# Optimization experiments

Hardware: AMD Instinct MI355X
Metric: run time of the kernel (lower is better)

Reference implementation:

```python
import jax, jax.numpy as jnp
import numpy as np
from jax import lax

B = 1024
D_VQ = 64
KS = 1024
KX = 1024
BETA = 0.25


def _conv1d(x, w, b):
    # x: [N, Cin, L], w: [Cout, Cin, 3], 'same' padding
    y = lax.conv_general_dilated(x, w, (1,), [(1, 1)], dimension_numbers=('NCH', 'OIH', 'NCH'))
    return y + b[None, :, None]


def _conv2d(x, w, b):
    # x: [N, Cin, H, W], w: [Cout, Cin, 3, 3], 'same' padding
    y = lax.conv_general_dilated(x, w, (1, 1), [(1, 1), (1, 1)], dimension_numbers=('NCHW', 'OIHW', 'NCHW'))
    return y + b[None, :, None, None]


def _gelu(x):
    return jax.nn.gelu(x, approximate=False)


def _vq_ema(z_e, codebook, beta):
    # z_e: [N, D], codebook: [K, D]
    d = (jnp.sum(z_e * z_e, axis=1, keepdims=True)
         - 2.0 * (z_e @ codebook.T)
         + jnp.sum(codebook * codebook, axis=1)[None, :])  # [N, K]
    idx = jnp.argmin(d, axis=1)                              # [N]
    z_q = codebook[idx]                                      # gather [N, D]
    vq_loss = beta * jnp.mean((z_e - lax.stop_gradient(z_q)) ** 2)
    z_q_st = z_e + lax.stop_gradient(z_q - z_e)              # straight-through
    n = z_e.shape[0]
    probs = jnp.zeros((codebook.shape[0],), z_e.dtype).at[idx].add(1.0) / n
    perplexity = jnp.exp(-jnp.sum(probs * jnp.log(probs + 1e-10)))
    return z_q_st, idx, vq_loss, perplexity


def setup_inputs() -> dict:
    key = jax.random.key(0)
    ks = iter(jax.random.split(key, 40))

    def p(shape, s=0.05):
        return jax.random.normal(next(ks), shape, jnp.float32) * s

    inp = {
        'cubes': jax.random.normal(next(ks), (B, 9, 8, 72), jnp.float32),
        # spectral encoder
        's_w1': p((16, 1, 3)), 's_b1': jnp.zeros((16,), jnp.float32),
        's_w2': p((16, 16, 3)), 's_b2': jnp.zeros((16,), jnp.float32),
        's_fc_w': p((D_VQ, 16 * 8)), 's_fc_b': jnp.zeros((D_VQ,), jnp.float32),
        'cb_s': p((KS, D_VQ), 1.0),
        # spectral decoder
        's_dec_fc_w': p((16 * 8, D_VQ)), 's_dec_fc_b': jnp.zeros((16 * 8,), jnp.float32),
        's_dec_w1': p((16, 16, 3)), 's_dec_b1': jnp.zeros((16,), jnp.float32),
        's_dec_w2': p((1, 16, 3)), 's_dec_b2': jnp.zeros((1,), jnp.float32),
        # spatial encoder
        'x_w1': p((16, 8, 3, 3)), 'x_b1': jnp.zeros((16,), jnp.float32),
        'x_w2': p((16, 16, 3, 3)), 'x_b2': jnp.zeros((16,), jnp.float32),
        'x_fc_w': p((D_VQ, 16 * 3 * 3)), 'x_fc_b': jnp.zeros((D_VQ,), jnp.float32),
        'cb_x': p((KX, D_VQ), 1.0),
        # spatial decoder
        'x_dec_fc_w': p((16 * 3 * 3, D_VQ)), 'x_dec_fc_b': jnp.zeros((16 * 3 * 3,), jnp.float32),
        'x_dec_w1': p((16, 16, 3, 3)), 'x_dec_b1': jnp.zeros((16,), jnp.float32),
        'x_dec_w2': p((8, 16, 3, 3)), 'x_dec_b2': jnp.zeros((8,), jnp.float32),
        'return_recon': 1,
    }
    return inp


def reference(cubes, s_w1, s_b1, s_w2, s_b2, s_fc_w, s_fc_b, cb_s,
              s_dec_fc_w, s_dec_fc_b, s_dec_w1, s_dec_b1, s_dec_w2, s_dec_b2,
              x_w1, x_b1, x_w2, x_b2, x_fc_w, x_fc_b, cb_x,
              x_dec_fc_w, x_dec_fc_b, x_dec_w1, x_dec_b1, x_dec_w2, x_dec_b2,
              return_recon):
    b, p, t, f = cubes.shape
    n = b * p * t
    c6 = cubes.reshape(b, p, t, 8, 3, 3)                   # [B,P,T,8,3,3]
    cperm = jnp.transpose(c6, (0, 1, 2, 4, 5, 3))          # [B,P,T,3,3,8]

    # --- spectral path ---
    spec = jnp.mean(cperm, axis=(3, 4))                    # [B,P,T,8]
    spec_seq = spec.reshape(n, 1, 8)
    s = _gelu(_conv1d(spec_seq, s_w1, s_b1))
    s = _gelu(_conv1d(s, s_w2, s_b2))
    z_e_s = s.reshape(n, 16 * 8) @ s_fc_w.T + s_fc_b       # [N,D]
    z_q_s, k_idx, vq_loss_s, perplex_s = _vq_ema(z_e_s, cb_s, BETA)
    emb_s = z_q_s.reshape(b, p, t, D_VQ)
    k_idx = k_idx.reshape(b, p, t)

    # --- spatial path ---
    spatial = c6.reshape(n, 8, 3, 3)
    x = _gelu(_conv2d(spatial, x_w1, x_b1))
    x = _gelu(_conv2d(x, x_w2, x_b2))
    z_e_x = x.reshape(n, 16 * 9) @ x_fc_w.T + x_fc_b
    z_q_x, m_idx, vq_loss_x, perplex_x = _vq_ema(z_e_x, cb_x, BETA)
    emb_x = z_q_x.reshape(b, p, t, D_VQ)
    m_idx = m_idx.reshape(b, p, t)

    total = vq_loss_s + vq_loss_x

    if return_recon:
        s_dec = (z_q_s @ s_dec_fc_w.T + s_dec_fc_b).reshape(n, 16, 8)
        s_dec = _gelu(_conv1d(s_dec, s_dec_w1, s_dec_b1))
        recon_s = _conv1d(s_dec, s_dec_w2, s_dec_b2)[:, 0, :].reshape(b, p, t, 8)
        recon_loss_s = jnp.mean((recon_s - spec) ** 2)

        x_dec = (z_q_x @ x_dec_fc_w.T + x_dec_fc_b).reshape(n, 16, 3, 3)
        x_dec = _gelu(_conv2d(x_dec, x_dec_w1, x_dec_b1))
        recon_x = _conv2d(x_dec, x_dec_w2, x_dec_b2)        # [N,8,3,3]
        recon_loss_x = jnp.mean((recon_x - spatial) ** 2)
        recon_loss_total = recon_loss_s + recon_loss_x
    else:
        recon_loss_total = jnp.float32(0.0)

    return (emb_s, emb_x, k_idx, m_idx, total, perplex_s, perplex_x, recon_loss_total)
```

## Files before the change

### kernel.cpp

```cpp
#include <hip/hip_runtime.h>
#include <math.h>

#define NTOK 73728

__device__ __forceinline__ float gelu_f(float x) {
    return 0.5f * x * (1.0f + erff(x * 0.70710678118654752440f));
}

__global__ void __launch_bounds__(256) k_prep(
    const float* __restrict__ cb_s, const float* __restrict__ cb_x,
    double* __restrict__ cn_s, double* __restrict__ cn_x,
    const float* __restrict__ s_dw1, const float* __restrict__ s_db1,
    const float* __restrict__ s_dfcw, const float* __restrict__ s_dfcb,
    float* __restrict__ weffT_s, float* __restrict__ beff_s,
    const float* __restrict__ x_dw1, const float* __restrict__ x_db1,
    const float* __restrict__ x_dfcw, const float* __restrict__ x_dfcb,
    float* __restrict__ weffT_x, float* __restrict__ beff_x,
    const float* __restrict__ s_fcw, float* __restrict__ fcwT_s,
    const float* __restrict__ x_fcw, float* __restrict__ fcwT_x,
    const float* __restrict__ s_w2, float* __restrict__ sw2T,
    const float* __restrict__ x_w1, float* __restrict__ xw1T,
    const float* __restrict__ x_w2, float* __restrict__ xw2T,
    const float* __restrict__ x_dw2, float* __restrict__ xdw2T)
{
// ... 60 lines not shown
            beff_x[o] = (float)bb;
        }
    } else if (bid < 108) {
        int i = (bid - 76) * 256 + tid;
        fcwT_s[i] = s_fcw[(i & 63) * 128 + (i >> 6)];
    } else if (bid < 144) {
        int i = (bid - 108) * 256 + tid;
        fcwT_x[i] = x_fcw[(i & 63) * 144 + (i >> 6)];
    } else {
        int i = (bid - 144) * 256 + tid;
        if (i < 768) {
            int c = i & 15, r = i >> 4;
            int ci = r / 3, dd = r % 3;
            sw2T[i] = s_w2[(c * 16 + ci) * 3 + dd];
        } else if (i < 1920) {
            int j = i - 768;
            int c = j & 15, r = j >> 4;
            int ci = r / 9, tap = r % 9;
            xw1T[j] = x_w1[(c * 8 + ci) * 9 + tap];
        } else if (i < 4224) {
            int j = i - 1920;
            int c = j & 15, r = j >> 4;
            int ci = r / 9, tap = r % 9;
            xw2T[j] = x_w2[(c * 16 + ci) * 9 + tap];
        } else {
            int j = i - 4224;
            int co = j & 7, r = j >> 3;
            int ci = r / 9, tap = r % 9;
            xdw2T[j] = x_dw2[(co * 16 + ci) * 9 + tap];
        }
    }
}

__global__ void __launch_bounds__(256) k_enc(
    const float* __restrict__ cubes,
    const float* __restrict__ s_w1, const float* __restrict__ s_b1,
    const float* __restrict__ sw2T, const float* __restrict__ s_b2,
    const float* __restrict__ fcwT_s, const float* __restrict__ s_fcb,
    float* __restrict__ emb_s,
    const float* __restrict__ xw1T, const float* __restrict__ x_b1,
    const float* __restrict__ xw2T, const float* __restrict__ x_b2,
    const float* __restrict__ fcwT_x, const float* __restrict__ x_fcb,
    float* __restrict__ emb_x)
{
    __shared__ float U[6528];
    int tid = threadIdx.x;
    int t = tid >> 4, c = tid & 15;
    if (blockIdx.x < 4608) {
        int b = blockIdx.x;
        float* S = U;
        float* A = U + 128;
        float* Bb = U + 2304;
        if (tid < 128) {
            int tk = tid >> 3, f = tid & 7;
            const float* cu = cubes + ((size_t)b * 16 + tk) * 72 + f * 9;
            float s = 0.f;
            #pragma unroll
            for (int k = 0; k < 9; ++k) s += cu[k];
            S[tk * 8 + f] = s * (1.0f / 9.0f);
        }
        __syncthreads();
        {
            float s0[8];
            *(float4*)&s0[0] = *(const float4*)&S[t * 8];
            *(float4*)&s0[4] = *(const float4*)&S[t * 8 + 4];
            float wa = s_w1[c * 3 + 0], wb = s_w1[c * 3 + 1], wc = s_w1[c * 3 + 2], bb = s_b1[c];
            #pragma unroll
            for (int l = 0; l < 8; ++l) {
                float v = fmaf(wb, s0[l], bb);
                if (l > 0) v = fmaf(wa, s0[l - 1], v);
                if (l < 7) v = fmaf(wc, s0[l + 1], v);
                A[t * 136 + c * 8 + l] = gelu_f(v);
            }
        }
        __syncthreads();
        {
            float acc[8];
            #pragma unroll
            for (int l = 0; l < 8; ++l) acc[l] = s_b2[c];
            for (int ci = 0; ci < 16; ++ci) {
                float r[8];
                *(float4*)&r[0] = *(const float4*)&A[t * 136 + ci * 8];
                *(float4*)&r[4] = *(const float4*)&A[t * 136 + ci * 8 + 4];
                float wa = sw2T[(ci * 3 + 0) * 16 + c];
                float wb = sw2T[(ci * 3 + 1) * 16 + c];
                float wc = sw2T[(ci * 3 + 2) * 16 + c];
                #pragma unroll
                for (int l = 0; l < 8; ++l) {
                    if (l > 0) acc[l] = fmaf(wa, r[l - 1], acc[l]);
                    acc[l] = fmaf(wb, r[l], acc[l]);
                    if (l < 7) acc[l] = fmaf(wc, r[l + 1], acc[l]);
                }
            }
            #pragma unroll
            for (int l = 0; l < 8; ++l) Bb[t * 136 + c * 8 + l] = gelu_f(acc[l]);
        }
        __syncthreads();
        {
            float4 zv = make_float4(s_fcb[c * 4 + 0], s_fcb[c * 4 + 1], s_fcb[c * 4 + 2], s_fcb[c * 4 + 3]);
            #pragma unroll 4
            for (int e = 0; e < 128; ++e) {
                float be = Bb[t * 136 + e];
                float4 wv = *(const float4*)(fcwT_s + (e << 6) + (c << 2));
                zv.x = fmaf(wv.x, be, zv.x);
                zv.y = fmaf(wv.y, be, zv.y);
                zv.z = fmaf(wv.z, be, zv.z);
                zv.w = fmaf(wv.w, be, zv.w);
            }
            *(float4*)(emb_s + ((size_t)b * 16 + t) * 64 + c * 4) = zv;
        }
    } else {
        int b = blockIdx.x - 4608;
        float* A = U;
        float* Bb = U + 3200;
        for (int u = tid; u < 1152; u += 256) {
            int tk = u / 72, e = u - tk * 72;
            int ci = e / 9, p = e - ci * 9;
            A[tk * 200 + ci * 12 + p] = cubes[(size_t)b * 1152 + u];
        }
        __syncthreads();
        {
            float acc[9];
            #pragma unroll
            for (int p = 0; p < 9; ++p) acc[p] = x_b1[c];
            for (int ci = 0; ci < 8; ++ci) {
                float r[12];
                *(float4*)&r[0] = *(const float4*)&A[t * 200 + ci * 12];
                *(float4*)&r[4] = *(const float4*)&A[t * 200 + ci * 12 + 4];
                *(float4*)&r[8] = *(const float4*)&A[t * 200 + ci * 12 + 8];
                float wv[9];
                #pragma unroll
                for (int q = 0; q < 9; ++q) wv[q] = xw1T[(ci * 9 + q) * 16 + c];
                #pragma unroll
                for (int p = 0; p < 9; ++p) {
                    int i = p / 3, j = p % 3;
                    #pragma unroll
                    for (int di = 0; di < 3; ++di) {
                        int ii = i + di - 1; if (ii < 0 || ii > 2) continue;
                        #pragma unroll
                        for (int dj = 0; dj < 3; ++dj) {
                            int jj = j + dj - 1; if (jj < 0 || jj > 2) continue;
                            acc[p] = fmaf(wv[di * 3 + dj], r[ii * 3 + jj], acc[p]);
                        }
                    }
                }
            }
            #pragma unroll
            for (int p = 0; p < 9; ++p) Bb[t * 200 + c * 12 + p] = gelu_f(acc[p]);
        }
        __syncthreads();
        {
            float acc[9];
            #pragma unroll
            for (int p = 0; p < 9; ++p) acc[p] = x_b2[c];
            for (int ci = 0; ci < 16; ++ci) {
                float r[12];
                *(float4*)&r[0] = *(const float4*)&Bb[t * 200 + ci * 12];
                *(float4*)&r[4] = *(const float4*)&Bb[t * 200 + ci * 12 + 4];
                *(float4*)&r[8] = *(const float4*)&Bb[t * 200 + ci * 12 + 8];
                float wv[9];
                #pragma unroll
                for (int q = 0; q < 9; ++q) wv[q] = xw2T[(ci * 9 + q) * 16 + c];
                #pragma unroll
                for (int p = 0; p < 9; ++p) {
                    int i = p / 3, j = p % 3;
                    #pragma unroll
                    for (int di = 0; di < 3; ++di) {
                        int ii = i + di - 1; if (ii < 0 || ii > 2) continue;
                        #pragma unroll
                        for (int dj = 0; dj < 3; ++dj) {
                            int jj = j + dj - 1; if (jj < 0 || jj > 2) continue;
                            acc[p] = fmaf(wv[di * 3 + dj], r[ii * 3 + jj], acc[p]);
                        }
                    }
                }
            }
            __syncthreads();
            #pragma unroll
            for (int p = 0; p < 9; ++p) A[t * 200 + c * 12 + p] = gelu_f(acc[p]);
        }
        __syncthreads();
        {
            float4 zv = make_float4(x_fcb[c * 4 + 0], x_fcb[c * 4 + 1], x_fcb[c * 4 + 2], x_fcb[c * 4 + 3]);
            #pragma unroll 4
            for (int e = 0; e < 144; ++e) {
                int ci = e / 9, p = e - ci * 9;
                float be = A[t * 200 + ci * 12 + p];
                float4 wv = *(const float4*)(fcwT_x + (e << 6) + (c << 2));
                zv.x = fmaf(wv.x, be, zv.x);
                zv.y = fmaf(wv.y, be, zv.y);
                zv.z = fmaf(wv.z, be, zv.z);
                zv.w = fmaf(wv.w, be, zv.w);
            }
            *(float4*)(emb_x + ((size_t)b * 16 + t) * 64 + c * 4) = zv;
        }
    }
}

__global__ void __launch_bounds__(256) k_vq(
    float* __restrict__ emb_s, float* __restrict__ emb_x,
    const float* __restrict__ cb_s, const float* __restrict__ cb_x,
    const double* __restrict__ cn_s, const double* __restrict__ cn_x,
    float* __restrict__ kidx, float* __restrict__ midx,
    int* __restrict__ hist_s, int* __restrict__ hist_x,
    double* __restrict__ p_vq_s, double* __restrict__ p_vq_x)
{
    __shared__ double pbest[4][64];
    __shared__ int pidx[4][64];
    __shared__ int lh[1024];
    int blk = blockIdx.x;
    int path = (blk >= 1152) ? 1 : 0;
    int b = blk - (path << 10) - (path << 7);
    float* emb = path ? emb_x : emb_s;
    const float* cb = path ? cb_x : cb_s;
    const double* cn = path ? cn_x : cn_s;
    float* idx_out = path ? midx : kidx;
    int* hist = path ? hist_x : hist_s;
    double* partial = path ? p_vq_x : p_vq_s;

    int tid = threadIdx.x;
    int w = tid >> 6, l = tid & 63;
    for (int u = tid; u < 1024; u += 256) lh[u] = 0;
    size_t n = (size_t)b * 64 + l;
    float z[64];
    {
        const float4* zp = (const float4*)(emb + n * 64);
        #pragma unroll
        for (int k = 0; k < 16; ++k) *(float4*)&z[k * 4] = zp[k];
    }
    int base = __builtin_amdgcn_readfirstlane(w << 8);
    const float* crb = cb + ((size_t)base << 6);
    const double* cnb = cn + base;
    double best = 1e300; int bi = base;
    for (int cc = 0; cc < 256; ++cc) {
        const float* cr = crb + (cc << 6);
        float d0 = 0.f, d1 = 0.f, d2 = 0.f, d3 = 0.f;
        #pragma unroll
        for (int k = 0; k < 64; k += 4) {
            d0 = fmaf(z[k + 0], cr[k + 0], d0);
            d1 = fmaf(z[k + 1], cr[k + 1], d1);
            d2 = fmaf(z[k + 2], cr[k + 2], d2);
            d3 = fmaf(z[k + 3], cr[k + 3], d3);
        }
        float dot = (d0 + d1) + (d2 + d3);
        double dd = cnb[cc] - 2.0 * (double)dot;
        if (dd < best) { best = dd; bi = base + cc; }
    }
    pbest[w][l] = best; pidx[w][l] = bi;
    __syncthreads();
    if (w == 0) {
        double bB = pbest[0][l]; int bj = pidx[0][l];
        #pragma unroll
        for (int q = 1; q < 4; ++q) {
            double d = pbest[q][l];
            if (d < bB) { bB = d; bj = pidx[q][l]; }
        }
        idx_out[n] = (float)bj;
        float qv[64];
        {
            const float4* cq = (const float4*)(cb + ((size_t)bj << 6));
            #pragma unroll
            for (int k = 0; k < 16; ++k) *(float4*)&qv[k * 4] = cq[k];
        }
        float vs = 0.f;
        #pragma unroll
        for (int k = 0; k < 64; ++k) { float df = z[k] - qv[k]; vs = fmaf(df, df, vs); }
        float4* zo = (float4*)(emb + n * 64);
        #pragma unroll
        for (int k = 0; k < 16; ++k) zo[k] = *(float4*)&qv[k * 4];
        atomicAdd(&lh[bj], 1);
        double s = (double)vs;
        #pragma unroll
        for (int o = 32; o > 0; o >>= 1) s += __shfl_down(s, o);
        if (l == 0) partial[b] = s;
    }
    __syncthreads();
    for (int u = tid; u < 1024; u += 256) if (lh[u] > 0) atomicAdd(&hist[u], lh[u]);
}

__global__ void __launch_bounds__(256) k_dec(
    const float* __restrict__ emb_s, const float* __restrict__ emb_x,
    const float* __restrict__ cubes,
    const float* __restrict__ weffT_s, const float* __restrict__ beff_s,
    const float* __restrict__ s_dw2, const float* __restrict__ s_db2,
    const float* __restrict__ weffT_x, const float* __restrict__ beff_x,
    const float* __restrict__ xdw2T, const float* __restrict__ x_db2,
    double* __restrict__ p_rec_s, double* __restrict__ p_rec_x)
{
    __shared__ float U[6016];
    __shared__ double wred[4];
    int tid = threadIdx.x;
    int t = tid >> 4, c = tid & 15;
    if (blockIdx.x < 4608) {
        int b = blockIdx.x;
        float* Z = U;
        float* Bb = U + 1152;
        float* S = U + 3328;
        {
            int tk = tid >> 4, dq = tid & 15;
            *(float4*)&Z[tk * 72 + dq * 4] =
                *(const float4*)(emb_s + (size_t)b * 1024 + (size_t)tid * 4);
        }
        if (tid < 128) {
            int tk = tid >> 3, f = tid & 7;
            const float* cu = cubes + ((size_t)b * 16 + tk) * 72 + f * 9;
            float s = 0.f;
            #pragma unroll
            for (int k = 0; k < 9; ++k) s += cu[k];
            S[tk * 8 + f] = s * (1.0f / 9.0f);
        }
        __syncthreads();
        {
            float4 a0 = make_float4(0.f, 0.f, 0.f, 0.f);
            float4 a1 = make_float4(0.f, 0.f, 0.f, 0.f);
            #pragma unroll 8
            for (int k = 0; k < 64; ++k) {
                float zk = Z[t * 72 + k];
                float4 w0 = *(const float4*)(weffT_s + k * 132 + (c << 2));
                float4 w1v = *(const float4*)(weffT_s + k * 132 + 64 + (c << 2));
                a0.x = fmaf(w0.x, zk, a0.x); a0.y = fmaf(w0.y, zk, a0.y);
                a0.z = fmaf(w0.z, zk, a0.z); a0.w = fmaf(w0.w, zk, a0.w);
                a1.x = fmaf(w1v.x, zk, a1.x); a1.y = fmaf(w1v.y, zk, a1.y);
                a1.z = fmaf(w1v.z, zk, a1.z); a1.w = fmaf(w1v.w, zk, a1.w);
            }
            int o0 = c << 2, o1 = 64 + (c << 2);
            float4 g0 = make_float4(gelu_f(a0.x + beff_s[o0 + 0]), gelu_f(a0.y + beff_s[o0 + 1]),
                                    gelu_f(a0.z + beff_s[o0 + 2]), gelu_f(a0.w + beff_s[o0 + 3]));
            float4 g1 = make_float4(gelu_f(a1.x + beff_s[o1 + 0]), gelu_f(a1.y + beff_s[o1 + 1]),
                                    gelu_f(a1.z + beff_s[o1 + 2]), gelu_f(a1.w + beff_s[o1 + 3]));
            *(float4*)&Bb[t * 136 + o0] = g0;
            *(float4*)&Bb[t * 136 + o1] = g1;
        }
        __syncthreads();
        float acc2 = 0.f;
        {
            int h = c >> 3, pos = c & 7;
            float a = (h == 0) ? s_db2[0] : 0.f;
            for (int ci = h * 8; ci < h * 8 + 8; ++ci) {
                const float* w = s_dw2 + ci * 3;
                const float* hb = &Bb[t * 136 + ci * 8];
                if (pos > 0) a = fmaf(w[0], hb[pos - 1], a);
                a = fmaf(w[1], hb[pos], a);
                if (pos < 7) a = fmaf(w[2], hb[pos + 1], a);
            }
            a += __shfl_xor(a, 8);
            if (h == 0) { float df = a - S[t * 8 + pos]; acc2 = df * df; }
        }
        double s = (double)acc2;
        #pragma unroll
        for (int o = 32; o > 0; o >>= 1) s += __shfl_down(s, o);
        if ((tid & 63) == 0) wred[tid >> 6] = s;
        __syncthreads();
        if (tid == 0) p_rec_s[b] = wred[0] + wred[1] + wred[2] + wred[3];
    } else {
        int b = blockIdx.x - 4608;
        float* Z = U;
        float* H = U + 1152;
        float* T = U + 4352;
        {
            int tk = tid >> 4, dq = tid & 15;
            *(float4*)&Z[tk * 72 + dq * 4] =
                *(const float4*)(emb_x + (size_t)b * 1024 + (size_t)tid * 4);
        }
        for (int u = tid; u < 1152; u += 256) {
            int tk = u / 72, e = u - tk * 72;
            int ci = e / 9, p = e - ci * 9;
            T[tk * 104 + ci * 12 + p] = cubes[(size_t)b * 1152 + u];
        }
        __syncthreads();
        {
            float4 a0 = make_float4(0.f, 0.f, 0.f, 0.f);
            float4 a1 = make_float4(0.f, 0.f, 0.f, 0.f);
            float4 a2 = make_float4(0.f, 0.f, 0.f, 0.f);
            #pragma unroll 8
            for (int k = 0; k < 64; ++k) {
                float zk = Z[t * 72 + k];
                float4 w0 = *(const float4*)(weffT_x + k * 148 + (c << 2));
                float4 w1v = *(const float4*)(weffT_x + k * 148 + 64 + (c << 2));
                float4 w2v = *(const float4*)(weffT_x + k * 148 + 128 + (c << 2));
                a0.x = fmaf(w0.x, zk, a0.x); a0.y = fmaf(w0.y, zk, a0.y);
                a0.z = fmaf(w0.z, zk, a0.z); a0.w = fmaf(w0.w, zk, a0.w);
                a1.x = fmaf(w1v.x, zk, a1.x); a1.y = fmaf(w1v.y, zk, a1.y);
                a1.z = fmaf(w1v.z, zk, a1.z); a1.w = fmaf(w1v.w, zk, a1.w);
                a2.x = fmaf(w2v.x, zk, a2.x); a2.y = fmaf(w2v.y, zk, a2.y);
                a2.z = fmaf(w2v.z, zk, a2.z); a2.w = fmaf(w2v.w, zk, a2.w);
            }
            float av[12] = {a0.x, a0.y, a0.z, a0.w, a1.x, a1.y, a1.z, a1.w, a2.x, a2.y, a2.z, a2.w};
            #pragma unroll
            for (int q = 0; q < 12; ++q) {
                int o = (c << 2) + ((q >> 2) << 6) + (q & 3);
                int ch = o / 9, p = o - ch * 9;
                H[t * 200 + ch * 12 + p] = gelu_f(av[q] + beff_x[o]);
            }
        }
        __syncthreads();
        float acc2 = 0.f;
        {
            int co = c >> 1, h = c & 1;
            float accp[9];
            #pragma unroll
            for (int p = 0; p < 9; ++p) accp[p] = (h == 0) ? x_db2[co] : 0.f;
            for (int ci = h * 8; ci < h * 8 + 8; ++ci) {
                float r[12];
                *(float4*)&r[0] = *(const float4*)&H[t * 200 + ci * 12];
                *(float4*)&r[4] = *(const float4*)&H[t * 200 + ci * 12 + 4];
                *(float4*)&r[8] = *(const float4*)&H[t * 200 + ci * 12 + 8];
                float wv[9];
                #pragma unroll
                for (int q = 0; q < 9; ++q) wv[q] = xdw2T[(ci * 9 + q) * 8 + co];
                #pragma unroll
                for (int p = 0; p < 9; ++p) {
                    int i = p / 3, j = p % 3;
                    #pragma unroll
                    for (int di = 0; di < 3; ++di) {
                        int ii = i + di - 1; if (ii < 0 || ii > 2) continue;
                        #pragma unroll
                        for (int dj = 0; dj < 3; ++dj) {
                            int jj = j + dj - 1; if (jj < 0 || jj > 2) continue;
                            accp[p] = fmaf(wv[di * 3 + dj], r[ii * 3 + jj], accp[p]);
                        }
                    }
                }
            }
            #pragma unroll
            for (int p = 0; p < 9; ++p) {
                float tot = accp[p] + __shfl_xor(accp[p], 1);
                if (h == 0) { float df = tot - T[t * 104 + co * 12 + p]; acc2 = fmaf(df, df, acc2); }
            }
        }
        double s = (double)acc2;
        #pragma unroll
        for (int o = 32; o > 0; o >>= 1) s += __shfl_down(s, o);
        if ((tid & 63) == 0) wred[tid >> 6] = s;
        __syncthreads();
        if (tid == 0) p_rec_x[b] = wred[0] + wred[1] + wred[2] + wred[3];
    }
}

__global__ void __launch_bounds__(256) k_final(
    const double* __restrict__ p_vq_s, const double* __restrict__ p_vq_x,
    const double* __restrict__ p_rec_s, const double* __restrict__ p_rec_x,
    const int* __restrict__ hist_s, const int* __restrict__ hist_x,
    const int* __restrict__ rr,
    float* __restrict__ outscal)
{
    __shared__ double wred[4];
    int tid = threadIdx.x;
    auto bred = [&](double v) -> double {
        #pragma unroll
        for (int o = 32; o > 0; o >>= 1) v += __shfl_down(v, o);
        __syncthreads();
        if ((tid & 63) == 0) wred[tid >> 6] = v;
        __syncthreads();
        return wred[0] + wred[1] + wred[2] + wred[3];
    };
    double a;
    a = 0; for (int t = tid; t < 1152; t += 256) a += p_vq_s[t];
    double vq_s = bred(a);
    a = 0; for (int t = tid; t < 1152; t += 256) a += p_vq_x[t];
    double vq_x = bred(a);
    a = 0; for (int t = tid; t < 4608; t += 256) a += p_rec_s[t];
    double rec_s = bred(a);
    a = 0; for (int t = tid; t < 4608; t += 256) a += p_rec_x[t];
    double rec_x = bred(a);
    a = 0;
    for (int t = tid; t < 1024; t += 256) {
        double cnt = (double)hist_s[t];
        if (cnt > 0.0) { double p = cnt / (double)NTOK; a += p * log(p + 1e-10); }
    }
// ... 50 lines not shown
    float* out   = (float*)d_out;
    float* emb_s = out;
    float* emb_x = out + 4718592;
    float* kidx  = out + 9437184;
    float* midx  = out + 9510912;
    float* scal  = out + 9584640;

    char* ws = (char*)d_ws;
    int*    hist_s  = (int*)(ws + 0);
    int*    hist_x  = (int*)(ws + 4096);
    double* cn_s    = (double*)(ws + 8192);
    double* cn_x    = (double*)(ws + 16384);
    double* p_vq_s  = (double*)(ws + 24576);
    double* p_vq_x  = (double*)(ws + 33792);
    double* p_rec_s = (double*)(ws + 43008);
    double* p_rec_x = (double*)(ws + 79872);
    float*  beff_s  = (float*)(ws + 116736);
    float*  beff_x  = (float*)(ws + 117248);
    float*  weffT_s = (float*)(ws + 117824);
    float*  weffT_x = (float*)(ws + 151616);
    float*  fcwT_s  = (float*)(ws + 189504);
    float*  fcwT_x  = (float*)(ws + 222272);
    float*  sw2T    = (float*)(ws + 259136);
    float*  xw1T    = (float*)(ws + 262208);
    float*  xw2T    = (float*)(ws + 266816);
    float*  xdw2T   = (float*)(ws + 276032);

    hipMemsetAsync(d_ws, 0, 8192, stream);
    k_prep<<<165, 256, 0, stream>>>(cb_s, cb_x, cn_s, cn_x,
                                    s_dw1, s_db1, s_dfcw, s_dfcb, weffT_s, beff_s,
                                    x_dw1, x_db1, x_dfcw, x_dfcb, weffT_x, beff_x,
                                    s_fcw, fcwT_s, x_fcw, fcwT_x,
                                    s_w2, sw2T, x_w1, xw1T, x_w2, xw2T, x_dw2, xdw2T);
    k_enc<<<9216, 256, 0, stream>>>(cubes, s_w1, s_b1, sw2T, s_b2, fcwT_s, s_fcb, emb_s,
                                    xw1T, x_b1, xw2T, x_b2, fcwT_x, x_fcb, emb_x);
    k_vq<<<2304, 256, 0, stream>>>(emb_s, emb_x, cb_s, cb_x, cn_s, cn_x,
                                   kidx, midx, hist_s, hist_x, p_vq_s, p_vq_x);
    k_dec<<<9216, 256, 0, stream>>>(emb_s, emb_x, cubes,
                                    weffT_s, beff_s, s_dw2, s_db2,
                                    weffT_x, beff_x, xdw2T, x_db2,
                                    p_rec_s, p_rec_x);
    k_final<<<1, 256, 0, stream>>>(p_vq_s, p_vq_x, p_rec_s, p_rec_x, hist_s, hist_x, rr, scal);
}
```

Before: 883.1 us.

## Reschedule stages into four kernels interleaving VQ with encoder/decoder work

Splits the combined encoder, VQ and decoder kernels into per-path bodies. It then regroups them into four launches: spectral encode, spatial encode interleaved with spectral VQ, spectral decode interleaved with spatial VQ, and spatial decode. The aim is to overlap the compute-heavy VQ argmin with the lighter conv work in the same launch and to cut per-kernel shared memory so more blocks fit on each CU. It adds one kernel launch and a 4:1 block-mixing scheme whose balance depends on the relative cost of each body.

```diff
diff --git a/kernel.cpp b/kernel.cpp
--- a/kernel.cpp
+++ b/kernel.cpp
@@ -116,193 +116,179 @@
     }
 }
 
-__global__ void __launch_bounds__(256) k_enc(
+__device__ void body_enc_spec(int b, int tid, float* U,
     const float* __restrict__ cubes,
-    const float* __restrict__ s_w1, const float* __restrict__ s_b1,
-    const float* __restrict__ sw2T, const float* __restrict__ s_b2,
-    const float* __restrict__ fcwT_s, const float* __restrict__ s_fcb,
-    float* __restrict__ emb_s,
-    const float* __restrict__ xw1T, const float* __restrict__ x_b1,
-    const float* __restrict__ xw2T, const float* __restrict__ x_b2,
-    const float* __restrict__ fcwT_x, const float* __restrict__ x_fcb,
-    float* __restrict__ emb_x)
-{
-    __shared__ float U[6528];
-    int tid = threadIdx.x;
+    const float* __restrict__ w1, const float* __restrict__ b1,
+    const float* __restrict__ sw2T, const float* __restrict__ b2,
+    const float* __restrict__ fcwT, const float* __restrict__ fcb,
+    float* __restrict__ emb)
+{
     int t = tid >> 4, c = tid & 15;
-    if (blockIdx.x < 4608) {
-        int b = blockIdx.x;
-        float* S = U;
-        float* A = U + 128;
-        float* Bb = U + 2304;
-        if (tid < 128) {
-            int tk = tid >> 3, f = tid & 7;
-            const float* cu = cubes + ((size_t)b * 16 + tk) * 72 + f * 9;
-            float s = 0.f;
-            #pragma unroll
-            for (int k = 0; k < 9; ++k) s += cu[k];
-            S[tk * 8 + f] = s * (1.0f / 9.0f);
-        }
-        __syncthreads();
-        {
-            float s0[8];
-            *(float4*)&s0[0] = *(const float4*)&S[t * 8];
-            *(float4*)&s0[4] = *(const float4*)&S[t * 8 + 4];
-            float wa = s_w1[c * 3 + 0], wb = s_w1[c * 3 + 1], wc = s_w1[c * 3 + 2], bb = s_b1[c];
+    float* S = U;
+    float* A = U + 128;
+    float* Bb = U + 2304;
+    if (tid < 128) {
+        int tk = tid >> 3, f = tid & 7;
+        const float* cu = cubes + ((size_t)b * 16 + tk) * 72 + f * 9;
+        float s = 0.f;
+        #pragma unroll
+        for (int k = 0; k < 9; ++k) s += cu[k];
+        S[tk * 8 + f] = s * (1.0f / 9.0f);
+    }
+    __syncthreads();
+    {
+        float s0[8];
+        *(float4*)&s0[0] = *(const float4*)&S[t * 8];
+        *(float4*)&s0[4] = *(const float4*)&S[t * 8 + 4];
+        float wa = w1[c * 3 + 0], wb = w1[c * 3 + 1], wc = w1[c * 3 + 2], bb = b1[c];
+        #pragma unroll
+        for (int l = 0; l < 8; ++l) {
+            float v = fmaf(wb, s0[l], bb);
+            if (l > 0) v = fmaf(wa, s0[l - 1], v);
+            if (l < 7) v = fmaf(wc, s0[l + 1], v);
+            A[t * 136 + c * 8 + l] = gelu_f(v);
+        }
+    }
+    __syncthreads();
+    {
+        float acc[8];
+        #pragma unroll
+        for (int l = 0; l < 8; ++l) acc[l] = b2[c];
+        for (int ci = 0; ci < 16; ++ci) {
+            float r[8];
+            *(float4*)&r[0] = *(const float4*)&A[t * 136 + ci * 8];
+            *(float4*)&r[4] = *(const float4*)&A[t * 136 + ci * 8 + 4];
+            float wa = sw2T[(ci * 3 + 0) * 16 + c];
+            float wb = sw2T[(ci * 3 + 1) * 16 + c];
+            float wc = sw2T[(ci * 3 + 2) * 16 + c];
             #pragma unroll
             for (int l = 0; l < 8; ++l) {
-                float v = fmaf(wb, s0[l], bb);
-                if (l > 0) v = fmaf(wa, s0[l - 1], v);
-                if (l < 7) v = fmaf(wc, s0[l + 1], v);
-                A[t * 136 + c * 8 + l] = gelu_f(v);
+                if (l > 0) acc[l] = fmaf(wa, r[l - 1], acc[l]);
+                acc[l] = fmaf(wb, r[l], acc[l]);
+                if (l < 7) acc[l] = fmaf(wc, r[l + 1], acc[l]);
             }
         }
-        __syncthreads();
-        {
-            float acc[8];
-            #pragma unroll
-            for (int l = 0; l < 8; ++l) acc[l] = s_b2[c];
-            for (int ci = 0; ci < 16; ++ci) {
-                float r[8];
-                *(float4*)&r[0] = *(const float4*)&A[t * 136 + ci * 8];
-                *(float4*)&r[4] = *(const float4*)&A[t * 136 + ci * 8 + 4];
-                float wa = sw2T[(ci * 3 + 0) * 16 + c];
-                float wb = sw2T[(ci * 3 + 1) * 16 + c];
-                float wc = sw2T[(ci * 3 + 2) * 16 + c];
+        #pragma unroll
+        for (int l = 0; l < 8; ++l) Bb[t * 136 + c * 8 + l] = gelu_f(acc[l]);
+    }
+    __syncthreads();
+    {
+        float4 zv = make_float4(fcb[c * 4 + 0], fcb[c * 4 + 1], fcb[c * 4 + 2], fcb[c * 4 + 3]);
+        #pragma unroll 4
+        for (int e = 0; e < 128; ++e) {
+            float be = Bb[t * 136 + e];
+            float4 wv = *(const float4*)(fcwT + (e << 6) + (c << 2));
+            zv.x = fmaf(wv.x, be, zv.x);
+            zv.y = fmaf(wv.y, be, zv.y);
+            zv.z = fmaf(wv.z, be, zv.z);
+            zv.w = fmaf(wv.w, be, zv.w);
+        }
+        *(float4*)(emb + ((size_t)b * 16 + t) * 64 + c * 4) = zv;
+    }
+}
+
+__device__ void body_enc_spat(int b, int tid, float* U,
+    const float* __restrict__ cubes,
+    const float* __restrict__ xw1T, const float* __restrict__ b1,
+    const float* __restrict__ xw2T, const float* __restrict__ b2,
+    const float* __restrict__ fcwT, const float* __restrict__ fcb,
+    float* __restrict__ emb)
+{
+    int t = tid >> 4, c = tid & 15;
+    float* A = U;
+    float* Bb = U + 3200;
+    for (int u = tid; u < 1152; u += 256) {
+        int tk = u / 72, e = u - tk * 72;
+        int ci = e / 9, p = e - ci * 9;
+        A[tk * 200 + ci * 12 + p] = cubes[(size_t)b * 1152 + u];
+    }
+    __syncthreads();
+    {
+        float acc[9];
+        #pragma unroll
+        for (int p = 0; p < 9; ++p) acc[p] = b1[c];
+        for (int ci = 0; ci < 8; ++ci) {
+            float r[12];
+            *(float4*)&r[0] = *(const float4*)&A[t * 200 + ci * 12];
+            *(float4*)&r[4] = *(const float4*)&A[t * 200 + ci * 12 + 4];
+            *(float4*)&r[8] = *(const float4*)&A[t * 200 + ci * 12 + 8];
+            float wv[9];
+            #pragma unroll
+            for (int q = 0; q < 9; ++q) wv[q] = xw1T[(ci * 9 + q) * 16 + c];
+            #pragma unroll
+            for (int p = 0; p < 9; ++p) {
+                int i = p / 3, j = p % 3;
                 #pragma unroll
-                for (int l = 0; l < 8; ++l) {
-                    if (l > 0) acc[l] = fmaf(wa, r[l - 1], acc[l]);
-                    acc[l] = fmaf(wb, r[l], acc[l]);
-                    if (l < 7) acc[l] = fmaf(wc, r[l + 1], acc[l]);
-                }
-            }
-            #pragma unroll
-            for (int l = 0; l < 8; ++l) Bb[t * 136 + c * 8 + l] = gelu_f(acc[l]);
-        }
-        __syncthreads();
-        {
-            float4 zv = make_float4(s_fcb[c * 4 + 0], s_fcb[c * 4 + 1], s_fcb[c * 4 + 2], s_fcb[c * 4 + 3]);
-            #pragma unroll 4
-            for (int e = 0; e < 128; ++e) {
-                float be = Bb[t * 136 + e];
-                float4 wv = *(const float4*)(fcwT_s + (e << 6) + (c << 2));
-                zv.x = fmaf(wv.x, be, zv.x);
-                zv.y = fmaf(wv.y, be, zv.y);
-                zv.z = fmaf(wv.z, be, zv.z);
-                zv.w = fmaf(wv.w, be, zv.w);
-            }
-            *(float4*)(emb_s + ((size_t)b * 16 + t) * 64 + c * 4) = zv;
-        }
-    } else {
-        int b = blockIdx.x - 4608;
-        float* A = U;
-        float* Bb = U + 3200;
-        for (int u = tid; u < 1152; u += 256) {
-            int tk = u / 72, e = u - tk * 72;
-            int ci = e / 9, p = e - ci * 9;
-            A[tk * 200 + ci * 12 + p] = cubes[(size_t)b * 1152 + u];
-        }
-        __syncthreads();
-        {
-            float acc[9];
-            #pragma unroll
-            for (int p = 0; p < 9; ++p) acc[p] = x_b1[c];
-            for (int ci = 0; ci < 8; ++ci) {
-                float r[12];
-                *(float4*)&r[0] = *(const float4*)&A[t * 200 + ci * 12];
-                *(float4*)&r[4] = *(const float4*)&A[t * 200 + ci * 12 + 4];
-                *(float4*)&r[8] = *(const float4*)&A[t * 200 + ci * 12 + 8];
-                float wv[9];
-                #pragma unroll
-                for (int q = 0; q < 9; ++q) wv[q] = xw1T[(ci * 9 + q) * 16 + c];
-                #pragma unroll
-                for (int p = 0; p < 9; ++p) {
-                    int i = p / 3, j = p % 3;
+                for (int di = 0; di < 3; ++di) {
+                    int ii = i + di - 1; if (ii < 0 || ii > 2) continue;
                     #pragma unroll
-                    for (int di = 0; di < 3; ++di) {
-                        int ii = i + di - 1; if (ii < 0 || ii > 2) continue;
-                        #pragma unroll
-                        for (int dj = 0; dj < 3; ++dj) {
-                            int jj = j + dj - 1; if (jj < 0 || jj > 2) continue;
-                            acc[p] = fmaf(wv[di * 3 + dj], r[ii * 3 + jj], acc[p]);
-                        }
+                    for (int dj = 0; dj < 3; ++dj) {
+                        int jj = j + dj - 1; if (jj < 0 || jj > 2) continue;
+                        acc[p] = fmaf(wv[di * 3 + dj], r[ii * 3 + jj], acc[p]);
                     }
                 }
             }
-            #pragma unroll
-            for (int p = 0; p < 9; ++p) Bb[t * 200 + c * 12 + p] = gelu_f(acc[p]);
-        }
-        __syncthreads();
-        {
-            float acc[9];
-            #pragma unroll
-            for (int p = 0; p < 9; ++p) acc[p] = x_b2[c];
-            for (int ci = 0; ci < 16; ++ci) {
-                float r[12];
-                *(float4*)&r[0] = *(const float4*)&Bb[t * 200 + ci * 12];
-                *(float4*)&r[4] = *(const float4*)&Bb[t * 200 + ci * 12 + 4];
-                *(float4*)&r[8] = *(const float4*)&Bb[t * 200 + ci * 12 + 8];
-                float wv[9];
+        }
+        #pragma unroll
+        for (int p = 0; p < 9; ++p) Bb[t * 200 + c * 12 + p] = gelu_f(acc[p]);
+    }
+    __syncthreads();
+    {
+        float acc[9];
+        #pragma unroll
+        for (int p = 0; p < 9; ++p) acc[p] = b2[c];
+        for (int ci = 0; ci < 16; ++ci) {
+            float r[12];
+            *(float4*)&r[0] = *(const float4*)&Bb[t * 200 + ci * 12];
+            *(float4*)&r[4] = *(const float4*)&Bb[t * 200 + ci * 12 + 4];
+            *(float4*)&r[8] = *(const float4*)&Bb[t * 200 + ci * 12 + 8];
+            float wv[9];
+            #pragma unroll
+            for (int q = 0; q < 9; ++q) wv[q] = xw2T[(ci * 9 + q) * 16 + c];
+            #pragma unroll
+            for (int p = 0; p < 9; ++p) {
+                int i = p / 3, j = p % 3;
                 #pragma unroll
-                for (int q = 0; q < 9; ++q) wv[q] = xw2T[(ci * 9 + q) * 16 + c];
-                #pragma unroll
-                for (int p = 0; p < 9; ++p) {
-                    int i = p / 3, j = p % 3;
+                for (int di = 0; di < 3; ++di) {
+                    int ii = i + di - 1; if (ii < 0 || ii > 2) continue;
                     #pragma unroll
-                    for (int di = 0; di < 3; ++di) {
-                        int ii = i + di - 1; if (ii < 0 || ii > 2) continue;
-                        #pragma unroll
-                        for (int dj = 0; dj < 3; ++dj) {
-                            int jj = j + dj - 1; if (jj < 0 || jj > 2) continue;
-                            acc[p] = fmaf(wv[di * 3 + dj], r[ii * 3 + jj], acc[p]);
-                        }
+                    for (int dj = 0; dj < 3; ++dj) {
+                        int jj = j + dj - 1; if (jj < 0 || jj > 2) continue;
+                        acc[p] = fmaf(wv[di * 3 + dj], r[ii * 3 + jj], acc[p]);
                     }
                 }
             }
-            __syncthreads();
-            #pragma unroll
-            for (int p = 0; p < 9; ++p) A[t * 200 + c * 12 + p] = gelu_f(acc[p]);
         }
         __syncthreads();
-        {
-            float4 zv = make_float4(x_fcb[c * 4 + 0], x_fcb[c * 4 + 1], x_fcb[c * 4 + 2], x_fcb[c * 4 + 3]);
-            #pragma unroll 4
-            for (int e = 0; e < 144; ++e) {
-                int ci = e / 9, p = e - ci * 9;
-                float be = A[t * 200 + ci * 12 + p];
-                float4 wv = *(const float4*)(fcwT_x + (e << 6) + (c << 2));
-                zv.x = fmaf(wv.x, be, zv.x);
-                zv.y = fmaf(wv.y, be, zv.y);
-                zv.z = fmaf(wv.z, be, zv.z);
-                zv.w = fmaf(wv.w, be, zv.w);
-            }
-            *(float4*)(emb_x + ((size_t)b * 16 + t) * 64 + c * 4) = zv;
-        }
-    }
-}
-
-__global__ void __launch_bounds__(256) k_vq(
-    float* __restrict__ emb_s, float* __restrict__ emb_x,
-    const float* __restrict__ cb_s, const float* __restrict__ cb_x,
-    const double* __restrict__ cn_s, const double* __restrict__ cn_x,
-    float* __restrict__ kidx, float* __restrict__ midx,
-    int* __restrict__ hist_s, int* __restrict__ hist_x,
-    double* __restrict__ p_vq_s, double* __restrict__ p_vq_x)
-{
-    __shared__ double pbest[4][64];
-    __shared__ int pidx[4][64];
-    __shared__ int lh[1024];
-    int blk = blockIdx.x;
-    int path = (blk >= 1152) ? 1 : 0;
-    int b = blk - (path << 10) - (path << 7);
-    float* emb = path ? emb_x : emb_s;
-    const float* cb = path ? cb_x : cb_s;
-    const double* cn = path ? cn_x : cn_s;
-    float* idx_out = path ? midx : kidx;
-    int* hist = path ? hist_x : hist_s;
-    double* partial = path ? p_vq_x : p_vq_s;
-
-    int tid = threadIdx.x;
+        #pragma unroll
+        for (int p = 0; p < 9; ++p) A[t * 200 + c * 12 + p] = gelu_f(acc[p]);
+    }
+    __syncthreads();
+    {
+        float4 zv = make_float4(fcb[c * 4 + 0], fcb[c * 4 + 1], fcb[c * 4 + 2], fcb[c * 4 + 3]);
+        #pragma unroll 4
+        for (int e = 0; e < 144; ++e) {
+            int ci = e / 9, p = e - ci * 9;
+            float be = A[t * 200 + ci * 12 + p];
+            float4 wv = *(const float4*)(fcwT + (e << 6) + (c << 2));
+            zv.x = fmaf(wv.x, be, zv.x);
+            zv.y = fmaf(wv.y, be, zv.y);
+            zv.z = fmaf(wv.z, be, zv.z);
+            zv.w = fmaf(wv.w, be, zv.w);
+        }
+        *(float4*)(emb + ((size_t)b * 16 + t) * 64 + c * 4) = zv;
+    }
+}
+
+__device__ void body_vq(int b, int tid, char* SMraw,
+    float* __restrict__ emb, const float* __restrict__ cb,
+    const double* __restrict__ cn,
+    float* __restrict__ idx_out, int* __restrict__ hist,
+    double* __restrict__ partial)
+{
+    double (*pbest)[64] = (double(*)[64])SMraw;
+    int (*pidx)[64] = (int(*)[64])(SMraw + 2048);
+    int* lh = (int*)(SMraw + 3072);
     int w = tid >> 6, l = tid & 63;
     for (int u = tid; u < 1024; u += 256) lh[u] = 0;
     size_t n = (size_t)b * 64 + l;
@@ -362,163 +348,225 @@
     for (int u = tid; u < 1024; u += 256) if (lh[u] > 0) atomicAdd(&hist[u], lh[u]);
 }
 
-__global__ void __launch_bounds__(256) k_dec(
-    const float* __restrict__ emb_s, const float* __restrict__ emb_x,
-    const float* __restrict__ cubes,
-    const float* __restrict__ weffT_s, const float* __restrict__ beff_s,
-    const float* __restrict__ s_dw2, const float* __restrict__ s_db2,
-    const float* __restrict__ weffT_x, const float* __restrict__ beff_x,
-    const float* __restrict__ xdw2T, const float* __restrict__ x_db2,
-    double* __restrict__ p_rec_s, double* __restrict__ p_rec_x)
-{
-    __shared__ float U[6016];
-    __shared__ double wred[4];
-    int tid = threadIdx.x;
+__device__ void body_dec_spec(int b, int tid, float* U, double* wred,
+    const float* __restrict__ emb, const float* __restrict__ cubes,
+    const float* __restrict__ weffT, const float* __restrict__ beff,
+    const float* __restrict__ dw2, const float* __restrict__ db2,
+    double* __restrict__ partial)
+{
     int t = tid >> 4, c = tid & 15;
-    if (blockIdx.x < 4608) {
-        int b = blockIdx.x;
-        float* Z = U;
-        float* Bb = U + 1152;
-        float* S = U + 3328;
-        {
-            int tk = tid >> 4, dq = tid & 15;
-            *(float4*)&Z[tk * 72 + dq * 4] =
-                *(const float4*)(emb_s + (size_t)b * 1024 + (size_t)tid * 4);
-        }
-        if (tid < 128) {
-            int tk = tid >> 3, f = tid & 7;
-            const float* cu = cubes + ((size_t)b * 16 + tk) * 72 + f * 9;
-            float s = 0.f;
-            #pragma unroll
-            for (int k = 0; k < 9; ++k) s += cu[k];
-            S[tk * 8 + f] = s * (1.0f / 9.0f);
-        }
-        __syncthreads();
-        {
-            float4 a0 = make_float4(0.f, 0.f, 0.f, 0.f);
-            float4 a1 = make_float4(0.f, 0.f, 0.f, 0.f);
-            #pragma unroll 8
-            for (int k = 0; k < 64; ++k) {
-                float zk = Z[t * 72 + k];
-                float4 w0 = *(const float4*)(weffT_s + k * 132 + (c << 2));
-                float4 w1v = *(const float4*)(weffT_s + k * 132 + 64 + (c << 2));
-                a0.x = fmaf(w0.x, zk, a0.x); a0.y = fmaf(w0.y, zk, a0.y);
-                a0.z = fmaf(w0.z, zk, a0.z); a0.w = fmaf(w0.w, zk, a0.w);
-                a1.x = fmaf(w1v.x, zk, a1.x); a1.y = fmaf(w1v.y, zk, a1.y);
-                a1.z = fmaf(w1v.z, zk, a1.z); a1.w = fmaf(w1v.w, zk, a1.w);
-            }
-            int o0 = c << 2, o1 = 64 + (c << 2);
-            float4 g0 = make_float4(gelu_f(a0.x + beff_s[o0 + 0]), gelu_f(a0.y + beff_s[o0 + 1]),
-                                    gelu_f(a0.z + beff_s[o0 + 2]), gelu_f(a0.w + beff_s[o0 + 3]));
-            float4 g1 = make_float4(gelu_f(a1.x + beff_s[o1 + 0]), gelu_f(a1.y + beff_s[o1 + 1]),
-                                    gelu_f(a1.z + beff_s[o1 + 2]), gelu_f(a1.w + beff_s[o1 + 3]));
-            *(float4*)&Bb[t * 136 + o0] = g0;
-            *(float4*)&Bb[t * 136 + o1] = g1;
-        }
-        __syncthreads();
-        float acc2 = 0.f;
-        {
-            int h = c >> 3, pos = c & 7;
-            float a = (h == 0) ? s_db2[0] : 0.f;
-            for (int ci = h * 8; ci < h * 8 + 8; ++ci) {
-                const float* w = s_dw2 + ci * 3;
-                const float* hb = &Bb[t * 136 + ci * 8];
-                if (pos > 0) a = fmaf(w[0], hb[pos - 1], a);
-                a = fmaf(w[1], hb[pos], a);
-                if (pos < 7) a = fmaf(w[2], hb[pos + 1], a);
-            }
-            a += __shfl_xor(a, 8);
-            if (h == 0) { float df = a - S[t * 8 + pos]; acc2 = df * df; }
-        }
-        double s = (double)acc2;
-        #pragma unroll
-        for (int o = 32; o > 0; o >>= 1) s += __shfl_down(s, o);
-        if ((tid & 63) == 0) wred[tid >> 6] = s;
-        __syncthreads();
-        if (tid == 0) p_rec_s[b] = wred[0] + wred[1] + wred[2] + wred[3];
-    } else {
-        int b = blockIdx.x - 4608;
-        float* Z = U;
-        float* H = U + 1152;
-        float* T = U + 4352;
-        {
-            int tk = tid >> 4, dq = tid & 15;
-            *(float4*)&Z[tk * 72 + dq * 4] =
-                *(const float4*)(emb_x + (size_t)b * 1024 + (size_t)tid * 4);
-        }
-        for (int u = tid; u < 1152; u += 256) {
-            int tk = u / 72, e = u - tk * 72;
-            int ci = e / 9, p = e - ci * 9;
-            T[tk * 104 + ci * 12 + p] = cubes[(size_t)b * 1152 + u];
-        }
-        __syncthreads();
-        {
-            float4 a0 = make_float4(0.f, 0.f, 0.f, 0.f);
-            float4 a1 = make_float4(0.f, 0.f, 0.f, 0.f);
-            float4 a2 = make_float4(0.f, 0.f, 0.f, 0.f);
-            #pragma unroll 8
-            for (int k = 0; k < 64; ++k) {
-                float zk = Z[t * 72 + k];
-                float4 w0 = *(const float4*)(weffT_x + k * 148 + (c << 2));
-                float4 w1v = *(const float4*)(weffT_x + k * 148 + 64 + (c << 2));
-                float4 w2v = *(const float4*)(weffT_x + k * 148 + 128 + (c << 2));
-                a0.x = fmaf(w0.x, zk, a0.x); a0.y = fmaf(w0.y, zk, a0.y);
-                a0.z = fmaf(w0.z, zk, a0.z); a0.w = fmaf(w0.w, zk, a0.w);
-                a1.x = fmaf(w1v.x, zk, a1.x); a1.y = fmaf(w1v.y, zk, a1.y);
-                a1.z = fmaf(w1v.z, zk, a1.z); a1.w = fmaf(w1v.w, zk, a1.w);
-                a2.x = fmaf(w2v.x, zk, a2.x); a2.y = fmaf(w2v.y, zk, a2.y);
-                a2.z = fmaf(w2v.z, zk, a2.z); a2.w = fmaf(w2v.w, zk, a2.w);
-            }
-            float av[12] = {a0.x, a0.y, a0.z, a0.w, a1.x, a1.y, a1.z, a1.w, a2.x, a2.y, a2.z, a2.w};
-            #pragma unroll
-            for (int q = 0; q < 12; ++q) {
-                int o = (c << 2) + ((q >> 2) << 6) + (q & 3);
-                int ch = o / 9, p = o - ch * 9;
-                H[t * 200 + ch * 12 + p] = gelu_f(av[q] + beff_x[o]);
-            }
-        }
-        __syncthreads();
-        float acc2 = 0.f;
-        {
-            int co = c >> 1, h = c & 1;
-            float accp[9];
-            #pragma unroll
-            for (int p = 0; p < 9; ++p) accp[p] = (h == 0) ? x_db2[co] : 0.f;
-            for (int ci = h * 8; ci < h * 8 + 8; ++ci) {
-                float r[12];
-                *(float4*)&r[0] = *(const float4*)&H[t * 200 + ci * 12];
-                *(float4*)&r[4] = *(const float4*)&H[t * 200 + ci * 12 + 4];
-                *(float4*)&r[8] = *(const float4*)&H[t * 200 + ci * 12 + 8];
-                float wv[9];
+    float* Z = U;
+    float* Bb = U + 1152;
+    float* S = U + 3328;
+    {
+        int tk = tid >> 4, dq = tid & 15;
+        *(float4*)&Z[tk * 72 + dq * 4] =
+            *(const float4*)(emb + (size_t)b * 1024 + (size_t)tid * 4);
+    }
+    if (tid < 128) {
+        int tk = tid >> 3, f = tid & 7;
+        const float* cu = cubes + ((size_t)b * 16 + tk) * 72 + f * 9;
+        float s = 0.f;
+        #pragma unroll
+        for (int k = 0; k < 9; ++k) s += cu[k];
+        S[tk * 8 + f] = s * (1.0f / 9.0f);
+    }
+    __syncthreads();
+    {
+        float4 a0 = make_float4(0.f, 0.f, 0.f, 0.f);
+        float4 a1 = make_float4(0.f, 0.f, 0.f, 0.f);
+        #pragma unroll 8
+        for (int k = 0; k < 64; ++k) {
+            float zk = Z[t * 72 + k];
+            float4 w0 = *(const float4*)(weffT + k * 132 + (c << 2));
+            float4 w1v = *(const float4*)(weffT + k * 132 + 64 + (c << 2));
+            a0.x = fmaf(w0.x, zk, a0.x); a0.y = fmaf(w0.y, zk, a0.y);
+            a0.z = fmaf(w0.z, zk, a0.z); a0.w = fmaf(w0.w, zk, a0.w);
+            a1.x = fmaf(w1v.x, zk, a1.x); a1.y = fmaf(w1v.y, zk, a1.y);
+            a1.z = fmaf(w1v.z, zk, a1.z); a1.w = fmaf(w1v.w, zk, a1.w);
+        }
+        int o0 = c << 2, o1 = 64 + (c << 2);
+        float4 g0 = make_float4(gelu_f(a0.x + beff[o0 + 0]), gelu_f(a0.y + beff[o0 + 1]),
+                                gelu_f(a0.z + beff[o0 + 2]), gelu_f(a0.w + beff[o0 + 3]));
+        float4 g1 = make_float4(gelu_f(a1.x + beff[o1 + 0]), gelu_f(a1.y + beff[o1 + 1]),
+                                gelu_f(a1.z + beff[o1 + 2]), gelu_f(a1.w + beff[o1 + 3]));
+        *(float4*)&Bb[t * 136 + o0] = g0;
+        *(float4*)&Bb[t * 136 + o1] = g1;
+    }
+    __syncthreads();
+    float acc2 = 0.f;
+    {
+        int h = c >> 3, pos = c & 7;
+        float a = (h == 0) ? db2[0] : 0.f;
+        for (int ci = h * 8; ci < h * 8 + 8; ++ci) {
+            const float* w = dw2 + ci * 3;
+            const float* hb = &Bb[t * 136 + ci * 8];
+            if (pos > 0) a = fmaf(w[0], hb[pos - 1], a);
+            a = fmaf(w[1], hb[pos], a);
+            if (pos < 7) a = fmaf(w[2], hb[pos + 1], a);
+        }
+        a += __shfl_xor(a, 8);
+        if (h == 0) { float df = a - S[t * 8 + pos]; acc2 = df * df; }
+    }
+    double s = (double)acc2;
+    #pragma unroll
+    for (int o = 32; o > 0; o >>= 1) s += __shfl_down(s, o);
+    if ((tid & 63) == 0) wred[tid >> 6] = s;
+    __syncthreads();
+    if (tid == 0) partial[b] = wred[0] + wred[1] + wred[2] + wred[3];
+}
+
+__device__ void body_dec_spat(int b, int tid, float* U, double* wred,
+    const float* __restrict__ emb, const float* __restrict__ cubes,
+    const float* __restrict__ weffT, const float* __restrict__ beff,
+    const float* __restrict__ xdw2T, const float* __restrict__ db2,
+    double* __restrict__ partial)
+{
+    int t = tid >> 4, c = tid & 15;
+    float* Z = U;
+    float* H = U + 1152;
+    float* T = U + 4352;
+    {
+        int tk = tid >> 4, dq = tid & 15;
+        *(float4*)&Z[tk * 72 + dq * 4] =
+            *(const float4*)(emb + (size_t)b * 1024 + (size_t)tid * 4);
+    }
+    for (int u = tid; u < 1152; u += 256) {
+        int tk = u / 72, e = u - tk * 72;
+        int ci = e / 9, p = e - ci * 9;
+        T[tk * 104 + ci * 12 + p] = cubes[(size_t)b * 1152 + u];
+    }
+    __syncthreads();
+    {
+        float4 a0 = make_float4(0.f, 0.f, 0.f, 0.f);
+        float4 a1 = make_float4(0.f, 0.f, 0.f, 0.f);
+        float4 a2 = make_float4(0.f, 0.f, 0.f, 0.f);
+        #pragma unroll 8
+        for (int k = 0; k < 64; ++k) {
+            float zk = Z[t * 72 + k];
+            float4 w0 = *(const float4*)(weffT + k * 148 + (c << 2));
+            float4 w1v = *(const float4*)(weffT + k * 148 + 64 + (c << 2));
+            float4 w2v = *(const float4*)(weffT + k * 148 + 128 + (c << 2));
+            a0.x = fmaf(w0.x, zk, a0.x); a0.y = fmaf(w0.y, zk, a0.y);
+            a0.z = fmaf(w0.z, zk, a0.z); a0.w = fmaf(w0.w, zk, a0.w);
+            a1.x = fmaf(w1v.x, zk, a1.x); a1.y = fmaf(w1v.y, zk, a1.y);
+            a1.z = fmaf(w1v.z, zk, a1.z); a1.w = fmaf(w1v.w, zk, a1.w);
+            a2.x = fmaf(w2v.x, zk, a2.x); a2.y = fmaf(w2v.y, zk, a2.y);
+            a2.z = fmaf(w2v.z, zk, a2.z); a2.w = fmaf(w2v.w, zk, a2.w);
+        }
+        float av[12] = {a0.x, a0.y, a0.z, a0.w, a1.x, a1.y, a1.z, a1.w, a2.x, a2.y, a2.z, a2.w};
+        #pragma unroll
+        for (int q = 0; q < 12; ++q) {
+            int o = (c << 2) + ((q >> 2) << 6) + (q & 3);
+            int ch = o / 9, p = o - ch * 9;
+            H[t * 200 + ch * 12 + p] = gelu_f(av[q] + beff[o]);
+        }
+    }
+    __syncthreads();
+    float acc2 = 0.f;
+    {
+        int co = c >> 1, h = c & 1;
+        float accp[9];
+        #pragma unroll
+        for (int p = 0; p < 9; ++p) accp[p] = (h == 0) ? db2[co] : 0.f;
+        for (int ci = h * 8; ci < h * 8 + 8; ++ci) {
+            float r[12];
+            *(float4*)&r[0] = *(const float4*)&H[t * 200 + ci * 12];
+            *(float4*)&r[4] = *(const float4*)&H[t * 200 + ci * 12 + 4];
+            *(float4*)&r[8] = *(const float4*)&H[t * 200 + ci * 12 + 8];
+            float wv[9];
+            #pragma unroll
+            for (int q = 0; q < 9; ++q) wv[q] = xdw2T[(ci * 9 + q) * 8 + co];
+            #pragma unroll
+            for (int p = 0; p < 9; ++p) {
+                int i = p / 3, j = p % 3;
                 #pragma unroll
-                for (int q = 0; q < 9; ++q) wv[q] = xdw2T[(ci * 9 + q) * 8 + co];
-                #pragma unroll
-                for (int p = 0; p < 9; ++p) {
-                    int i = p / 3, j = p % 3;
+                for (int di = 0; di < 3; ++di) {
+                    int ii = i + di - 1; if (ii < 0 || ii > 2) continue;
                     #pragma unroll
-                    for (int di = 0; di < 3; ++di) {
-                        int ii = i + di - 1; if (ii < 0 || ii > 2) continue;
-                        #pragma unroll
-                        for (int dj = 0; dj < 3; ++dj) {
-                            int jj = j + dj - 1; if (jj < 0 || jj > 2) continue;
-                            accp[p] = fmaf(wv[di * 3 + dj], r[ii * 3 + jj], accp[p]);
-                        }
+                    for (int dj = 0; dj < 3; ++dj) {
+                        int jj = j + dj - 1; if (jj < 0 || jj > 2) continue;
+                        accp[p] = fmaf(wv[di * 3 + dj], r[ii * 3 + jj], accp[p]);
                     }
                 }
             }
-            #pragma unroll
-            for (int p = 0; p < 9; ++p) {
-                float tot = accp[p] + __shfl_xor(accp[p], 1);
-                if (h == 0) { float df = tot - T[t * 104 + co * 12 + p]; acc2 = fmaf(df, df, acc2); }
-            }
-        }
-        double s = (double)acc2;
-        #pragma unroll
-        for (int o = 32; o > 0; o >>= 1) s += __shfl_down(s, o);
-        if ((tid & 63) == 0) wred[tid >> 6] = s;
-        __syncthreads();
-        if (tid == 0) p_rec_x[b] = wred[0] + wred[1] + wred[2] + wred[3];
-    }
+        }
+        #pragma unroll
+        for (int p = 0; p < 9; ++p) {
+            float tot = accp[p] + __shfl_xor(accp[p], 1);
+            if (h == 0) { float df = tot - T[t * 104 + co * 12 + p]; acc2 = fmaf(df, df, acc2); }
+        }
+    }
+    double s = (double)acc2;
+    #pragma unroll
+    for (int o = 32; o > 0; o >>= 1) s += __shfl_down(s, o);
+    if ((tid & 63) == 0) wred[tid >> 6] = s;
+    __syncthreads();
+    if (tid == 0) partial[b] = wred[0] + wred[1] + wred[2] + wred[3];
+}
+
+__global__ void __launch_bounds__(256) k1_enc_spec(
+    const float* __restrict__ cubes,
+    const float* __restrict__ s_w1, const float* __restrict__ s_b1,
+    const float* __restrict__ sw2T, const float* __restrict__ s_b2,
+    const float* __restrict__ fcwT_s, const float* __restrict__ s_fcb,
+    float* __restrict__ emb_s)
+{
+    __shared__ __align__(16) float U[4480];
+    body_enc_spec(blockIdx.x, threadIdx.x, U, cubes, s_w1, s_b1, sw2T, s_b2, fcwT_s, s_fcb, emb_s);
+}
+
+__global__ void __launch_bounds__(256) k2_encx_vqs(
+    const float* __restrict__ cubes,
+    const float* __restrict__ xw1T, const float* __restrict__ x_b1,
+    const float* __restrict__ xw2T, const float* __restrict__ x_b2,
+    const float* __restrict__ fcwT_x, const float* __restrict__ x_fcb,
+    float* __restrict__ emb_x,
+    float* __restrict__ emb_s, const float* __restrict__ cb_s,
+    const double* __restrict__ cn_s,
+    float* __restrict__ kidx, int* __restrict__ hist_s, double* __restrict__ p_vq_s)
+{
+    __shared__ __align__(16) char SM[25600];
+    int bid = blockIdx.x, tid = threadIdx.x;
+    if ((bid % 5) != 4) {
+        int b = (bid / 5) * 4 + (bid % 5);
+        body_enc_spat(b, tid, (float*)SM, cubes, xw1T, x_b1, xw2T, x_b2, fcwT_x, x_fcb, emb_x);
+    } else {
+        int b = bid / 5;
+        body_vq(b, tid, SM, emb_s, cb_s, cn_s, kidx, hist_s, p_vq_s);
+    }
+}
+
+__global__ void __launch_bounds__(256) k3_decs_vqx(
+    const float* __restrict__ emb_s, const float* __restrict__ cubes,
+    const float* __restrict__ weffT_s, const float* __restrict__ beff_s,
+    const float* __restrict__ s_dw2, const float* __restrict__ s_db2,
+    double* __restrict__ p_rec_s,
+    float* __restrict__ emb_x, const float* __restrict__ cb_x,
+    const double* __restrict__ cn_x,
+    float* __restrict__ midx, int* __restrict__ hist_x, double* __restrict__ p_vq_x)
+{
+    __shared__ __align__(16) char SM[13856];
+    __shared__ double wred[4];
+    int bid = blockIdx.x, tid = threadIdx.x;
+    if ((bid % 5) != 4) {
+        int b = (bid / 5) * 4 + (bid % 5);
+        body_dec_spec(b, tid, (float*)SM, wred, emb_s, cubes, weffT_s, beff_s, s_dw2, s_db2, p_rec_s);
+    } else {
+        int b = bid / 5;
+        body_vq(b, tid, SM, emb_x, cb_x, cn_x, midx, hist_x, p_vq_x);
+    }
+}
+
+__global__ void __launch_bounds__(256) k4_dec_spat(
+    const float* __restrict__ emb_x, const float* __restrict__ cubes,
+    const float* __restrict__ weffT_x, const float* __restrict__ beff_x,
+    const float* __restrict__ xdw2T, const float* __restrict__ x_db2,
+    double* __restrict__ p_rec_x)
+{
+    __shared__ __align__(16) float U[6016];
+    __shared__ double wred[4];
+    body_dec_spat(blockIdx.x, threadIdx.x, U, wred, emb_x, cubes, weffT_x, beff_x, xdw2T, x_db2, p_rec_x);
 }
 
 __global__ void __launch_bounds__(256) k_final(
@@ -635,13 +683,11 @@
                                     x_dw1, x_db1, x_dfcw, x_dfcb, weffT_x, beff_x,
                                     s_fcw, fcwT_s, x_fcw, fcwT_x,
                                     s_w2, sw2T, x_w1, xw1T, x_w2, xw2T, x_dw2, xdw2T);
-    k_enc<<<9216, 256, 0, stream>>>(cubes, s_w1, s_b1, sw2T, s_b2, fcwT_s, s_fcb, emb_s,
-                                    xw1T, x_b1, xw2T, x_b2, fcwT_x, x_fcb, emb_x);
-    k_vq<<<2304, 256, 0, stream>>>(emb_s, emb_x, cb_s, cb_x, cn_s, cn_x,
-                                   kidx, midx, hist_s, hist_x, p_vq_s, p_vq_x);
-    k_dec<<<9216, 256, 0, stream>>>(emb_s, emb_x, cubes,
-                                    weffT_s, beff_s, s_dw2, s_db2,
-                                    weffT_x, beff_x, xdw2T, x_db2,
-                                    p_rec_s, p_rec_x);
+    k1_enc_spec<<<4608, 256, 0, stream>>>(cubes, s_w1, s_b1, sw2T, s_b2, fcwT_s, s_fcb, emb_s);
+    k2_encx_vqs<<<5760, 256, 0, stream>>>(cubes, xw1T, x_b1, xw2T, x_b2, fcwT_x, x_fcb, emb_x,
+                                          emb_s, cb_s, cn_s, kidx, hist_s, p_vq_s);
+    k3_decs_vqx<<<5760, 256, 0, stream>>>(emb_s, cubes, weffT_s, beff_s, s_dw2, s_db2, p_rec_s,
+                                          emb_x, cb_x, cn_x, midx, hist_x, p_vq_x);
+    k4_dec_spat<<<4608, 256, 0, stream>>>(emb_x, cubes, weffT_x, beff_x, xdw2T, x_db2, p_rec_x);
     k_final<<<1, 256, 0, stream>>>(p_vq_s, p_vq_x, p_rec_s, p_rec_x, hist_s, hist_x, rr, scal);
 }
```

After: 1.962 ms. +122.2%, slower.
